# Kernel tuning notes

Measured on AMD Instinct MI355X. Metric: run time of the kernel, lower is better.

## Reference

```python
import jax, jax.numpy as jnp
import numpy as np

B, D, H = 1024, 128, 128
LN_EPS = 1e-5


def setup_inputs() -> dict:
    key = jax.random.key(0)
    ks = jax.random.split(key, 12)
    s_d = 1.0 / np.sqrt(D)
    s_h = 1.0 / np.sqrt(H)
    return {
        "x": jax.random.normal(ks[0], (B, D), dtype=jnp.float32),
        # diff_proj: Linear(D, H)
        "Wd": jax.random.uniform(ks[1], (H, D), jnp.float32, -s_d, s_d),
        "bd": jax.random.uniform(ks[2], (H,), jnp.float32, -s_d, s_d),
        # tau_proj: Linear(D, 1) -> Softplus
        "Wt": jax.random.uniform(ks[3], (1, D), jnp.float32, -s_d, s_d),
        "bt": jax.random.uniform(ks[4], (1,), jnp.float32, -s_d, s_d),
        # agg: Linear(H, H) -> ReLU
        "Wa": jax.random.uniform(ks[5], (H, H), jnp.float32, -s_h, s_h),
        "ba": jax.random.uniform(ks[6], (H,), jnp.float32, -s_h, s_h),
        # res_proj: Linear(D, H)
        "Wr": jax.random.uniform(ks[7], (H, D), jnp.float32, -s_d, s_d),
        "br": jax.random.uniform(ks[8], (H,), jnp.float32, -s_d, s_d),
        # LayerNorm(H)
        "gamma": jnp.ones((H,), jnp.float32),
        "beta": jnp.zeros((H,), jnp.float32),
    }


def reference(x, Wd, bd, Wt, bt, Wa, ba, Wr, br, gamma, beta):
    # mean_j diff_proj(|x_i - x_j|) == diff_proj(mean_j |x_i - x_j|) since Linear is affine
    diffs_mean = jnp.mean(jnp.abs(x[:, None, :] - x[None, :, :]), axis=1)  # [B, D]
    d_mean = diffs_mean @ Wd.T + bd                                         # [B, H]
    # tau = softplus(x Wt^T + bt).clamp(min=0.01) + 1.0
    tau = jnp.clip(jax.nn.softplus(x @ Wt.T + bt), 0.01, None) + 1.0        # [B, 1]
    h_mean = d_mean / tau
    h = jax.nn.relu(h_mean @ Wa.T + ba)
    y = h + x @ Wr.T + br
    mu = jnp.mean(y, axis=-1, keepdims=True)
    var = jnp.var(y, axis=-1, keepdims=True)
    return (y - mu) / jnp.sqrt(var + LN_EPS) * gamma + beta
```

## Files before the change

kernel.cpp:

```cpp
#include <hip/hip_runtime.h>
#include <math.h>

#define Bn 1024
#define Dn 128
#define Hn 128

__global__ __launch_bounds__(1024) void col_sort_dmean(
    const float* __restrict__ x, float* __restrict__ dmean) {
  const int d = blockIdx.x;
  const int t = threadIdx.x;

  __shared__ unsigned long long kvs[Bn];
  __shared__ float wsum[16];

  const float v0 = x[(size_t)t * Dn + d];
  const unsigned int u = __float_as_uint(v0);
  const unsigned int key = u ^ ((u >> 31) ? 0xFFFFFFFFu : 0x80000000u);
  unsigned long long kv = ((unsigned long long)key << 32) | (unsigned int)t;

#pragma unroll
  for (int k = 2; k <= Bn; k <<= 1) {
#pragma unroll
    for (int j = k >> 1; j > 0; j >>= 1) {
      unsigned long long other;
      if (j >= 64) {
        kvs[t] = kv;
        __syncthreads();
        other = kvs[t ^ j];
        __syncthreads();
      } else {
        other = __shfl_xor(kv, j, 64);
      }
      const bool up = ((t & k) == 0);
      const bool lowHalf = ((t & j) == 0);
      const bool keepMin = (up == lowHalf);
      const bool otherSmaller = (other < kv);
      if (keepMin == otherSmaller) kv = other;
    }
  }

  const unsigned int skey = (unsigned int)(kv >> 32);
  const unsigned int orig = (unsigned int)(kv & 0xFFFFFFFFu);
  const unsigned int ub =
      (skey & 0x80000000u) ? (skey ^ 0x80000000u) : ~skey;
  const float sv = __uint_as_float(ub);

  const int lane = t & 63;
  const int wv = t >> 6;
  float ps = sv;
#pragma unroll
  for (int off = 1; off < 64; off <<= 1) {
    const float n = __shfl_up(ps, off, 64);
    if (lane >= off) ps += n;
  }
  if (lane == 63) wsum[wv] = ps;
  __syncthreads();
  float woff = 0.f, tot = 0.f;
#pragma unroll
  for (int w = 0; w < 16; ++w) {
    const float s = wsum[w];
    tot += s;
    if (w < wv) woff += s;
  }
  const float pexcl = (ps - sv) + woff;

  const float res =
      ((float)(2 * t - Bn) * sv + tot - 2.0f * pexcl) * (1.0f / (float)Bn);
  dmean[(size_t)orig * Dn + d] = res;
}

__global__ __launch_bounds__(256) void fused_tail(
    const float* __restrict__ x, const float* __restrict__ dmean,
    const float* __restrict__ Wd, const float* __restrict__ bd,
    const float* __restrict__ Wt, const float* __restrict__ bt,
    const float* __restrict__ Wa, const float* __restrict__ ba,
    const float* __restrict__ Wr, const float* __restrict__ br,
    const float* __restrict__ gamma, const float* __restrict__ beta,
    float* __restrict__ out) {
  const int t = threadIdx.x;
  const int i0 = blockIdx.x << 2;

  __shared__ float xs[4][Dn];
  __shared__ float dms[4][Dn];
  __shared__ float ms[4][Hn];
  __shared__ float ys[4][Hn];
  __shared__ float wt_s[Dn];
  __shared__ float tau_s[4];

  {
    const int r = t >> 6, p2 = (t & 63) << 1;
    *(float2*)&xs[r][p2] = *(const float2*)(x + (size_t)(i0 + r) * Dn + p2);
    *(float2*)&dms[r][p2] =
        *(const float2*)(dmean + (size_t)(i0 + r) * Dn + p2);
    if (t < Dn) wt_s[t] = Wt[t];
  }
  __syncthreads();

  {
    const int r = t >> 6, p = t & 63;
    float partial = xs[r][p] * wt_s[p] + xs[r][p + 64] * wt_s[p + 64];
#pragma unroll
    for (int off = 32; off; off >>= 1) partial += __shfl_xor(partial, off, 64);
    if (p == 0) {
      const float z = partial + bt[0];
      const float sp = fmaxf(z, 0.f) + log1pf(expf(-fabsf(z)));
      tau_s[r] = 1.0f / (fmaxf(sp, 0.01f) + 1.0f);
    }
  }
  __syncthreads();

  {
    const int h = t & 127;
    const int g4 = t >> 7;
    const int r0 = 2 * g4, r1 = 2 * g4 + 1;
    float m0 = bd[h], m1 = m0;
    const float4* w = (const float4*)(Wd + (size_t)h * Dn);
#pragma unroll 4
    for (int k4 = 0; k4 < Dn / 4; ++k4) {
      const float4 wv = w[k4];
      const int k = k4 * 4;
      m0 += wv.x * dms[r0][k] + wv.y * dms[r0][k + 1] + wv.z * dms[r0][k + 2] +
            wv.w * dms[r0][k + 3];
      m1 += wv.x * dms[r1][k] + wv.y * dms[r1][k + 1] + wv.z * dms[r1][k + 2] +
            wv.w * dms[r1][k + 3];
    }
    ms[r0][h] = m0 * tau_s[r0];
    ms[r1][h] = m1 * tau_s[r1];
  }
  __syncthreads();

  {
    const int h = t & 127;
    const int g4 = t >> 7;
    const int r0 = 2 * g4, r1 = 2 * g4 + 1;
    float q0 = ba[h], q1 = q0, c0 = br[h], c1 = c0;
    const float4* wa = (const float4*)(Wa + (size_t)h * Dn);
    const float4* wr = (const float4*)(Wr + (size_t)h * Dn);
#pragma unroll 4
    for (int k4 = 0; k4 < Dn / 4; ++k4) {
      const float4 av = wa[k4];
      const float4 rv = wr[k4];
      const int k = k4 * 4;
      q0 += av.x * ms[r0][k] + av.y * ms[r0][k + 1] + av.z * ms[r0][k + 2] +
            av.w * ms[r0][k + 3];
      q1 += av.x * ms[r1][k] + av.y * ms[r1][k + 1] + av.z * ms[r1][k + 2] +
            av.w * ms[r1][k + 3];
      c0 += rv.x * xs[r0][k] + rv.y * xs[r0][k + 1] + rv.z * xs[r0][k + 2] +
            rv.w * xs[r0][k + 3];
      c1 += rv.x * xs[r1][k] + rv.y * xs[r1][k + 1] + rv.z * xs[r1][k + 2] +
            rv.w * xs[r1][k + 3];
    }
    ys[r0][h] = fmaxf(q0, 0.f) + c0;
    ys[r1][h] = fmaxf(q1, 0.f) + c1;
  }
  __syncthreads();

  {
    const int r = t >> 6, p = t & 63;
    const float v0 = ys[r][p], v1 = ys[r][p + 64];
    float s = v0 + v1;
    float q = v0 * v0 + v1 * v1;
#pragma unroll
    for (int off = 32; off; off >>= 1) {
      s += __shfl_xor(s, off, 64);
      q += __shfl_xor(q, off, 64);
    }
    const float mu = s * (1.0f / 128.0f);
    const float var = q * (1.0f / 128.0f) - mu * mu;
    const float rs = rsqrtf(var + 1e-5f);
    float* o = out + (size_t)(i0 + r) * Hn;
    o[p] = (v0 - mu) * rs * gamma[p] + beta[p];
    o[p + 64] = (v1 - mu) * rs * gamma[p + 64] + beta[p + 64];
  }
}

extern "C" void kernel_launch(void* const* d_in, const int* in_sizes, int n_in,
                              void* d_out, int out_size, void* d_ws,
                              size_t ws_size, hipStream_t stream) {
  const float* x = (const float*)d_in[0];
  const float* Wd = (const float*)d_in[1];
  const float* bd = (const float*)d_in[2];
  const float* Wt = (const float*)d_in[3];
  const float* bt = (const float*)d_in[4];
  const float* Wa = (const float*)d_in[5];
  const float* ba = (const float*)d_in[6];
  const float* Wr = (const float*)d_in[7];
  const float* br = (const float*)d_in[8];
  const float* gamma = (const float*)d_in[9];
  const float* beta = (const float*)d_in[10];
  float* out = (float*)d_out;
  float* dmean = (float*)d_ws;

  col_sort_dmean<<<Dn, Bn, 0, stream>>>(x, dmean);
  fused_tail<<<Bn / 4, 256, 0, stream>>>(x, dmean, Wd, bd, Wt, bt, Wa, ba, Wr,
                                         br, gamma, beta, out);
  (void)in_sizes; (void)n_in; (void)out_size; (void)ws_size;
}
```

Before: 100.2 us.

## Sort 32-bit keys only and recover ranks by binary search

```diff
diff --git a/kernel.cpp b/kernel.cpp
--- a/kernel.cpp
+++ b/kernel.cpp
@@ -10,39 +10,39 @@
   const int d = blockIdx.x;
   const int t = threadIdx.x;
 
-  __shared__ unsigned long long kvs[Bn];
+  __shared__ unsigned int kbuf[2][Bn];
+  __shared__ float pref_s[Bn];
   __shared__ float wsum[16];
 
   const float v0 = x[(size_t)t * Dn + d];
   const unsigned int u = __float_as_uint(v0);
-  const unsigned int key = u ^ ((u >> 31) ? 0xFFFFFFFFu : 0x80000000u);
-  unsigned long long kv = ((unsigned long long)key << 32) | (unsigned int)t;
-
+  const unsigned int mykey = u ^ ((u >> 31) ? 0xFFFFFFFFu : 0x80000000u);
+  unsigned int key = mykey;
+
+  int buf = 0;
 #pragma unroll
   for (int k = 2; k <= Bn; k <<= 1) {
 #pragma unroll
-    for (int j = k >> 1; j > 0; j >>= 1) {
-      unsigned long long other;
-      if (j >= 64) {
-        kvs[t] = kv;
-        __syncthreads();
-        other = kvs[t ^ j];
-        __syncthreads();
-      } else {
-        other = __shfl_xor(kv, j, 64);
-      }
-      const bool up = ((t & k) == 0);
-      const bool lowHalf = ((t & j) == 0);
-      const bool keepMin = (up == lowHalf);
-      const bool otherSmaller = (other < kv);
-      if (keepMin == otherSmaller) kv = other;
-    }
-  }
-
-  const unsigned int skey = (unsigned int)(kv >> 32);
-  const unsigned int orig = (unsigned int)(kv & 0xFFFFFFFFu);
-  const unsigned int ub =
-      (skey & 0x80000000u) ? (skey ^ 0x80000000u) : ~skey;
+    for (int j = k >> 1; j >= 64; j >>= 1) {
+      kbuf[buf][t] = key;
+      __syncthreads();
+      const unsigned int other = kbuf[buf][t ^ j];
+      buf ^= 1;
+      const bool keepMin = (((t & k) == 0) == ((t & j) == 0));
+      if ((other < key) == keepMin) key = other;
+    }
+    const int j0 = ((k >> 1) < 32) ? (k >> 1) : 32;
+#pragma unroll
+    for (int j = j0; j > 0; j >>= 1) {
+      const unsigned int other = (unsigned int)__shfl_xor((int)key, j, 64);
+      const bool keepMin = (((t & k) == 0) == ((t & j) == 0));
+      if ((other < key) == keepMin) key = other;
+    }
+  }
+
+  kbuf[0][t] = key;
+
+  const unsigned int ub = (key & 0x80000000u) ? (key ^ 0x80000000u) : ~key;
   const float sv = __uint_as_float(ub);
 
   const int lane = t & 63;
@@ -62,11 +62,19 @@
     tot += s;
     if (w < wv) woff += s;
   }
-  const float pexcl = (ps - sv) + woff;
+  pref_s[t] = (ps - sv) + woff;
+  __syncthreads();
+
+  unsigned int pos = 0;
+#pragma unroll
+  for (int s = 512; s > 0; s >>= 1) {
+    if (kbuf[0][pos + s - 1] < mykey) pos += s;
+  }
+  const float P = pref_s[pos];
 
   const float res =
-      ((float)(2 * t - Bn) * sv + tot - 2.0f * pexcl) * (1.0f / (float)Bn);
-  dmean[(size_t)orig * Dn + d] = res;
+      ((float)(2 * (int)pos - Bn) * v0 + tot - 2.0f * P) * (1.0f / (float)Bn);
+  dmean[(size_t)t * Dn + d] = res;
 }
 
 __global__ __launch_bounds__(256) void fused_tail(
```

Result: no change. 98.85 us (-1.3%).
